# Performance work log

Measured on AMD Instinct MI355X. Metric: run time of the kernel, lower is better.

The kernel has to match this reference:

```python
import jax, jax.numpy as jnp
import numpy as np

B, S, E, H = 4, 1024, 768, 12
DH = E // H  # per-head dim = 64
PRIOR_VAR = 0.01


def _kl(mu, logvar):
    # kl_regularizer from the source: logvar (units,) broadcasts against mu (in,units)
    t = (jnp.log(PRIOR_VAR) - 1.0 - logvar
         + jnp.log1p(jnp.exp(logvar)) / PRIOR_VAR
         + mu * mu / PRIOR_VAR)
    return 0.5 * jnp.mean(t)


def _linear_first(x, w_mu, w_sigma):
    mu = x @ w_mu
    W_Sigma = jnp.log1p(jnp.exp(w_sigma))            # softplus(w_sigma)
    xs = x / x.shape[-1]                              # x / dim (dim = last dim of x)
    xx = jnp.sum(xs * xs, axis=-1, keepdims=True)     # [B,S,1]
    Sigma = jax.nn.softplus(xx * W_Sigma)             # [B,S,E]
    return mu, Sigma, _kl(w_mu, w_sigma)


def _linear_not_first(mu_in, Sigma_in, w_mu, w_sigma):
    mu = mu_in @ w_mu
    W_Sigma = jnp.log1p(jnp.exp(w_sigma))
    wm = w_mu / jnp.sqrt(jnp.float32(w_mu.shape[0]))  # w_mu / sqrt(in_dim)
    S1 = Sigma_in @ (wm * wm)                         # w^T Sigma_in w
    xs = mu_in / mu_in.shape[-1]
    S2 = jnp.sum(xs * xs, axis=-1, keepdims=True) * W_Sigma
    S3 = jnp.sum(Sigma_in, axis=-1, keepdims=True) * W_Sigma / W_Sigma.shape[-1]
    Sigma = jax.nn.softplus(S1 + S2 + S3)
    return mu, Sigma, _kl(w_mu, w_sigma)


def _heads(x):
    # [B,S,E] -> [B,H,S,DH]
    return x.reshape(B, S, H, DH).transpose(0, 2, 1, 3)


def setup_inputs() -> dict:
    key = jax.random.key(0)
    ks = jax.random.split(key, 9)
    glorot = lambda k: jax.random.normal(k, (E, E), jnp.float32) * jnp.sqrt(2.0 / (E + E))
    sig = lambda k: jax.random.uniform(k, (E,), jnp.float32, minval=-4.6, maxval=-2.25)
    return {
        "x": jax.random.normal(ks[0], (B, S, E), jnp.float32),
        "wq_mu": glorot(ks[1]), "wq_sigma": sig(ks[2]),
        "wk_mu": glorot(ks[3]), "wk_sigma": sig(ks[4]),
        "wv_mu": glorot(ks[5]), "wv_sigma": sig(ks[6]),
        "wo_mu": glorot(ks[7]), "wo_sigma": sig(ks[8]),
    }


def reference(x, wq_mu, wq_sigma, wk_mu, wk_sigma, wv_mu, wv_sigma, wo_mu, wo_sigma):
    # dropout is identity in eval mode (training=False)
    mq, sq, klq = _linear_first(x, wq_mu, wq_sigma)
    mk, sk, klk = _linear_first(x, wk_mu, wk_sigma)
    mv, sv, klv = _linear_first(x, wv_mu, wv_sigma)
    mq, sq, mk, sk, mv, sv = map(_heads, (mq, sq, mk, sk, mv, sv))

    dk = jnp.float32(DH)
    mu_score = jnp.einsum('bhqd,bhkd->bhqk', mq, mk)
    a = jnp.einsum('bhqd,bhkd->bhqk', mq * mq / dk, sk)
    b = jnp.einsum('bhqd,bhkd->bhqk', mk * mk / dk, sq)   # matmul(mk^2/dk, sq^T) as in TF source
    c = jnp.einsum('bhqd,bhkd->bhqk', sq / jnp.sqrt(dk), sk / jnp.sqrt(dk))
    sigma_score = a + b + c

    mu_scaled = mu_score / jnp.sqrt(dk)
    sigma_scaled = sigma_score / dk
    w = jax.nn.softmax(mu_scaled, axis=-1)               # [B,H,S,S]
    wd = jnp.float32(S)
    grad = (w - w * w) ** 2
    Sw = grad * sigma_scaled / wd

    mu_att = jnp.einsum('bhqk,bhkd->bhqd', w, mv)
    d = jnp.einsum('bhqk,bhkd->bhqd', w * w / wd, sv)
    e = jnp.einsum('bhqk,bhkd->bhqd', Sw, mv * mv / wd)
    f = jnp.einsum('bhqk,bhkd->bhqd', Sw / jnp.sqrt(wd), sv / jnp.sqrt(wd))
    sig_att = jax.nn.softplus(d + e + f)

    mu_cat = mu_att.transpose(0, 2, 1, 3).reshape(B, S, E)
    sig_cat = sig_att.transpose(0, 2, 1, 3).reshape(B, S, E)

    mu_out, Sigma_out, klo = _linear_not_first(mu_cat, sig_cat, wo_mu, wo_sigma)
    Sigma_out = jax.nn.softplus(Sigma_out)               # extra softplus in call()
    kl = klq + klk + klv + klo
    return mu_out, Sigma_out, kl
```

## Files before the change

kernel.cpp:

```cpp
#include <hip/hip_runtime.h>
#include <math.h>

#define EN 768
#define SN 1024
#define HN 12
#define BSN 4096
#define BSE 3145728

typedef __attribute__((ext_vector_type(8))) short bf16x8;
typedef __attribute__((ext_vector_type(4))) float f32x4;
typedef __attribute__((ext_vector_type(4))) unsigned short u16x4;
typedef __attribute__((ext_vector_type(4))) unsigned int u32x4;
typedef unsigned short u16;

#define OFF_XX   0u
#define OFF_RC   16384u
#define OFF_WSIG 32768u
#define OFF_KL   45056u
#define OFF_ZI   49152u
#define OFF_WT   262144u
#define OFF_QH   4980736u
#define OFF_KH   11272192u
#define OFF_SQD  17563648u
#define OFF_SKD  23855104u
#define OFF_MVT  30146560u
#define OFF_MV2  36438016u
#define OFF_SVT  42729472u
#define OFF_MUH  49020928u
#define OFF_SGH  55312384u

__device__ __forceinline__ float sp_f(float x){
  return fmaxf(x, 0.f) + log1pf(__expf(-fabsf(x)));
}
__device__ __forceinline__ u16 f2b(float f){
  unsigned u = __float_as_uint(f);
  return (u16)((u + 0x7fffu + ((u>>16)&1u)) >> 16);
}
__device__ __forceinline__ float b2f(u16 h){
  return __uint_as_float(((unsigned)h)<<16);
}
__device__ __forceinline__ unsigned cvtpk(float lo, float hi){
  unsigned r;
  asm("v_cvt_pk_bf16_f32 %0, %1, %2" : "=v"(r) : "v"(lo), "v"(hi));
  return r;
}
__device__ __forceinline__ bf16x8 u2b(u32x4 v){
  union{u32x4 u; bf16x8 b;} x; x.u = v; return x.b;
}
__device__ __forceinline__ f32x4 mfma16(bf16x8 a, bf16x8 b, f32x4 c){
  return __builtin_amdgcn_mfma_f32_16x16x32_bf16(a, b, c, 0, 0, 0);
}
__device__ __forceinline__ bf16x8 sq8(bf16x8 a){
  union{bf16x8 b; u32x4 u;} x; x.b = a;
  u32x4 r;
  #pragma unroll
  for (int i=0;i<4;++i){
    unsigned v = x.u[i];
    float f0 = __uint_as_float(v<<16);
    float f1 = __uint_as_float(v & 0xffff0000u);
    r[i] = cvtpk(f0*f0, f1*f1);
  }
  return u2b(r);
}
__device__ __forceinline__ bf16x8 ldsr(const u16* t, int row, int sg){
  int a16 = (row<<3) + (sg ^ (row&7));
  return *(const bf16x8*)(t + (a16<<3));
}
__device__ __forceinline__ void stage64(u16* dst, const u16* src, int rstride, int tid){
  #pragma unroll
  for (int it=0; it<2; ++it){
    int idx = (it<<8) + tid;
    int row = idx>>3, seg = idx&7;
    bf16x8 v = *(const bf16x8*)(src + (long)row*rstride + (seg<<3));
    int a16 = (row<<3) + (seg ^ (row&7));
    *(bf16x8*)(dst + (a16<<3)) = v;
  }
}

__device__ __forceinline__ float blk_reduce(float v, float* tmp){
  #pragma unroll
  for (int off = 32; off; off >>= 1) v += __shfl_down(v, off, 64);
  int w = threadIdx.x >> 6;
  if ((threadIdx.x & 63) == 0) tmp[w] = v;
  __syncthreads();
  float r = 0.f;
  if (threadIdx.x == 0) r = tmp[0] + tmp[1] + tmp[2] + tmp[3];
  __syncthreads();
  return r;
}

__global__ void k_prep(const float* __restrict__ s0, const float* __restrict__ s1,
                       const float* __restrict__ s2, const float* __restrict__ s3,
                       float* __restrict__ wsig, float* __restrict__ klacc){
  __shared__ float tmp[4];
  const float* src = (blockIdx.x==0)?s0:(blockIdx.x==1)?s1:(blockIdx.x==2)?s2:s3;
  int l = blockIdx.x;
  float ssum=0.f, spsum=0.f;
  for (int j=threadIdx.x; j<EN; j+=256){
    float sg = src[j];
    float w  = log1pf(__expf(sg));
    wsig[l*EN+j] = w;
    ssum += sg; spsum += w;
  }
  float a = blk_reduce(ssum, tmp);
  float b = blk_reduce(spsum, tmp);
  if (threadIdx.x==0){ atomicAdd(&klacc[1], a); atomicAdd(&klacc[2], b); }
}

__global__ void k_xx(const float* __restrict__ x, float* __restrict__ xx){
  __shared__ float tmp[4];
  int r = blockIdx.x;
  const float* xr = x + (long)r*EN;
  float s=0.f;
  for (int j=threadIdx.x; j<EN; j+=256){ float v = xr[j]; s += v*v; }
  float t = blk_reduce(s, tmp);
  if (threadIdx.x==0) xx[r] = t*(1.0f/589824.0f);
}

__global__ void k_mu2(const float* __restrict__ w0, const float* __restrict__ w1,
                      const float* __restrict__ w2, const float* __restrict__ w3,
                      float* __restrict__ klacc){
  __shared__ float tmp[4];
  const float* w = (blockIdx.y==0)?w0:(blockIdx.y==1)?w1:(blockIdx.y==2)?w2:w3;
  const float4* w4 = (const float4*)w;
  float s=0.f;
  for (int i=blockIdx.x*256+threadIdx.x; i<147456; i+=gridDim.x*256){
    float4 v = w4[i];
    s += v.x*v.x + v.y*v.y + v.z*v.z + v.w*v.w;
  }
  float r = blk_reduce(s, tmp);
  if (threadIdx.x==0) atomicAdd(&klacc[0], r);
}

__global__ void k_wt(const float* __restrict__ w0, const float* __restrict__ w1,
                     const float* __restrict__ w2, const float* __restrict__ w3,
                     u16* __restrict__ wt){
  __shared__ float t[64*65];
  const float* W = (blockIdx.z==0)?w0:(blockIdx.z==1)?w1:(blockIdx.z==2)?w2:w3;
  u16* WT = wt + (long)blockIdx.z*589824;
  int r0 = blockIdx.y<<6, c0 = blockIdx.x<<6;
  int tid = threadIdx.x;
  #pragma unroll
  for (int it=0; it<16; ++it){
    int idx=(it<<8)+tid; int r=idx>>6, c=idx&63;
    t[c*65+r] = W[(long)(r0+r)*EN + c0+c];
  }
  __syncthreads();
  #pragma unroll
  for (int it=0; it<16; ++it){
    int idx=(it<<8)+tid; int c=idx>>6, r=idx&63;
    WT[(long)(c0+c)*EN + r0+r] = f2b(t[c*65+r]);
  }
}

__global__ void k_sigarr(const float* __restrict__ xx, const float* __restrict__ wsig,
                         u16* __restrict__ sqd, u16* __restrict__ skd){
  int r = blockIdx.x;
  float xr = xx[r];
  for (int c=threadIdx.x; c<EN; c+=256){
    sqd[(long)r*EN+c] = f2b(sp_f(xr*wsig[c])*(1.0f/64.0f));
    skd[(long)r*EN+c] = f2b(sp_f(xr*wsig[EN+c])*(1.0f/64.0f));
  }
}

__global__ void k_svt(const float* __restrict__ xx, const float* __restrict__ wsig,
                      u16* __restrict__ svT){
  __shared__ float sxx[64], swv[64];
  int kt=blockIdx.x, h=blockIdx.y, b=blockIdx.z, tid=threadIdx.x;
  if (tid < 64){
    sxx[tid] = xx[(long)b*SN + (kt<<6) + tid];
    swv[tid] = wsig[2*EN + (h<<6) + tid];
  }
  __syncthreads();
  long obase = (((long)(b*HN+h))<<6)*SN + (kt<<6);
  #pragma unroll
  for (int it=0; it<16; ++it){
    int idx=(it<<8)+tid; int d=idx>>6, k=idx&63;
    svT[obase + (long)d*SN + k] = f2b(sp_f(sxx[k]*swv[d]));
  }
}

__global__ __launch_bounds__(256)
void k_projmm(const float* __restrict__ x, const u16* __restrict__ WT,
              u16* __restrict__ oq, u16* __restrict__ ok,
              u16* __restrict__ mvT, u16* __restrict__ mv2T){
  __shared__ __align__(16) u16 lds[8192];
  u16* At = lds; u16* Bt = lds + 4096;
  const int tid = threadIdx.x;
  const int w = tid>>6, l = tid&63, l15 = l&15, g = l>>4;
  const int m0 = blockIdx.y<<6, n0 = blockIdx.x<<6;
  const u16* Wt = WT + (long)blockIdx.z*589824;
  f32x4 acc[4];
  #pragma unroll
  for (int t=0;t<4;++t){ acc[t][0]=0;acc[t][1]=0;acc[t][2]=0;acc[t][3]=0; }
  for (int k0=0; k0<EN; k0+=64){
    __syncthreads();
    #pragma unroll
    for (int it=0; it<2; ++it){
      int idx=(it<<8)+tid; int row=idx>>3, seg=idx&7;
      const float* sp = x + (long)(m0+row)*EN + k0 + (seg<<3);
      float4 a = *(const float4*)sp; float4 c = *(const float4*)(sp+4);
      bf16x8 v;
      v[0]=(short)f2b(a.x); v[1]=(short)f2b(a.y); v[2]=(short)f2b(a.z); v[3]=(short)f2b(a.w);
      v[4]=(short)f2b(c.x); v[5]=(short)f2b(c.y); v[6]=(short)f2b(c.z); v[7]=(short)f2b(c.w);
      int a16=(row<<3)+(seg^(row&7));
      *(bf16x8*)(At + (a16<<3)) = v;
    }
    stage64(Bt, Wt + (long)n0*EN + k0, EN, tid);
    __syncthreads();
    #pragma unroll
    for (int s=0;s<2;++s){
      int sg=(s<<2)+g;
      bf16x8 af = ldsr(At, (w<<4)+l15, sg);
      #pragma unroll
      for (int t=0;t<4;++t)
        acc[t] = mfma16(af, ldsr(Bt,(t<<4)+l15,sg), acc[t]);
    }
  }
  if (blockIdx.z < 2){
    u16* out = blockIdx.z ? ok : oq;
    #pragma unroll
    for (int t=0;t<4;++t){
      int col = n0 + (t<<4) + l15;
      #pragma unroll
      for (int r=0;r<4;++r){
        long row = m0 + (w<<4) + (g<<2) + r;
        out[row*EN + col] = f2b(acc[t][r]);
      }
    }
  } else {
    int b  = m0 >> 10;
    int hh = n0 >> 6;
    long obase = (((long)(b*HN+hh))<<6)*SN;
    int tok0 = (m0 & 1023) + (w<<4) + (g<<2);
    #pragma unroll
    for (int t=0;t<4;++t){
      int d = (t<<4) + l15;
      u16x4 m4, s4;
      #pragma unroll
      for (int r=0;r<4;++r){
        u16 mb = f2b(acc[t][r]);
        m4[r] = mb;
        float mf = b2f(mb);
        s4[r] = f2b(mf*mf);
      }
      *(u16x4*)&mvT[obase + (long)d*SN + tok0]  = m4;
      *(u16x4*)&mv2T[obase + (long)d*SN + tok0] = s4;
    }
  }
}

__global__ __launch_bounds__(512)
void k_z(const u16* __restrict__ qh, const u16* __restrict__ kh,
         float* __restrict__ zi){
  __shared__ __align__(16) u16 Tk[4096];
  const int tid = threadIdx.x;
  const int w = tid>>6, l = tid&63, l15 = l&15, g = l>>4;
  const int i = blockIdx.x;
  const int xcd = i & 7, slot = i >> 3;
  const int qt = slot & 7;
  const int pair = xcd*6 + (slot >> 3);
  const int h = pair % HN, b = pair / HN;
  const int q0 = qt<<7;
  const long bS = (long)b*SN;
  bf16x8 amq[2];
  {
    long qrow = (bS + q0 + (w<<4) + l15) * EN;
    #pragma unroll
    for (int s=0;s<2;++s)
      amq[s] = *(const bf16x8*)(qh + qrow + (h<<6) + (s<<5) + (g<<3));
  }
  const u16* khb = kh + bS*EN + (h<<6);
  const int srow = tid>>3, sseg = tid&7;
  const int a16o = (((srow<<3) + (sseg ^ (srow&7)))<<3);
  bf16x8 pf = *(const bf16x8*)(khb + (long)srow*EN + (sseg<<3));
  f32x4 zacc = {0.f,0.f,0.f,0.f};
  for (int kt=0; kt<16; ++kt){
    __syncthreads();
    *(bf16x8*)(Tk + a16o) = pf;
    __syncthreads();
    if (kt < 15)
      pf = *(const bf16x8*)(khb + (long)(((kt+1)<<6)+srow)*EN + (sseg<<3));
    f32x4 smu[4];
    #pragma unroll
    for (int t=0;t<4;++t){ smu[t][0]=0;smu[t][1]=0;smu[t][2]=0;smu[t][3]=0; }
    #pragma unroll
    for (int s=0;s<2;++s){
      int sg=(s<<2)+g;
      #pragma unroll
      for (int t=0;t<4;++t)
        smu[t] = mfma16(amq[s], ldsr(Tk,(t<<4)+l15,sg), smu[t]);
    }
    #pragma unroll
    for (int t=0;t<4;++t)
      #pragma unroll
      for (int r=0;r<4;++r)
        zacc[r] += __expf(smu[t][r]*0.125f);
  }
  #pragma unroll
  for (int m=1; m<16; m<<=1){
    #pragma unroll
    for (int r=0;r<4;++r) zacc[r] += __shfl_xor(zacc[r], m, 64);
  }
  if (l15 == 0){
    long zbase = (((long)(b*HN+h))<<10) + q0 + (w<<4) + (g<<2);
    #pragma unroll
    for (int r=0;r<4;++r) zi[zbase + r] = 1.0f/zacc[r];
  }
}

__global__ __launch_bounds__(512, 2)
void k_attn(const u16* __restrict__ qh, const u16* __restrict__ kh,
            const u16* __restrict__ sqd, const u16* __restrict__ skd,
            const u16* __restrict__ mvT, const u16* __restrict__ svT,
            const u16* __restrict__ mv2T, const float* __restrict__ zi,
            u16* __restrict__ muh, u16* __restrict__ sgh){
  extern __shared__ u16 lds2[];
  u16* Tk  = lds2;
  u16* Tsk = lds2 + 4096;
  u16* Tsq = lds2 + 8192;
  u16* Tmv = lds2 + 12288;
  u16* Tsv = lds2 + 16384;
  u16* Tm2 = lds2 + 20480;
  const int tid = threadIdx.x;
  const int w = tid>>6, l = tid&63, l15 = l&15, g = l>>4;
  unsigned* Pu = (unsigned*)(lds2 + 24576) + (w<<10);
  const int i = blockIdx.x;
  const int xcd = i & 7, slot = i >> 3;
  const int qt = slot & 7;
  const int pair = xcd*6 + (slot >> 3);
  const int h = pair % HN, b = pair / HN;
  const int q0 = qt<<7;
  const long bS = (long)b*SN;

  bf16x8 amq[2], acb[2], amk2[2];
  {
    long qrow = (bS + q0 + (w<<4) + l15) * EN;
    #pragma unroll
    for (int s=0;s<2;++s){
      int eoff = (h<<6) + (s<<5) + (g<<3);
      bf16x8 q8 = *(const bf16x8*)(qh + qrow + eoff);
      bf16x8 k8 = *(const bf16x8*)(kh + qrow + eoff);
      bf16x8 s8 = *(const bf16x8*)(sqd + qrow + eoff);
      amq[s] = q8;
      bf16x8 t2, tc;
      #pragma unroll
      for (int j=0;j<8;++j){
        float kv = b2f((u16)k8[j]);
        t2[j] = (short)f2b(kv*kv);
        float qv = b2f((u16)q8[j]);
        float sv = b2f((u16)s8[j]) * 64.0f;
        tc[j] = (short)f2b(qv*qv + sv);
      }
      amk2[s] = t2; acb[s] = tc;
    }
  }
  float zl[4];
  {
    long zbase = (((long)(b*HN+h))<<10) + q0 + (w<<4) + (g<<2);
    #pragma unroll
    for (int r=0;r<4;++r) zl[r] = zi[zbase + r];
  }

  const u16* khb = kh  + bS*EN + (h<<6);
  const u16* skb = skd + bS*EN + (h<<6);
  const u16* sqb = sqd + bS*EN + (h<<6);
  const long hb64 = ((long)(b*HN+h))<<6;
  const u16* mvb = mvT  + hb64*SN;
  const u16* svb = svT  + hb64*SN;
  const u16* m2b = mv2T + hb64*SN;

  f32x4 accM[4], acc2[4], acc3[4];
  #pragma unroll
  for (int t=0;t<4;++t){
    accM[t][0]=0;accM[t][1]=0;accM[t][2]=0;accM[t][3]=0;
    acc2[t][0]=0;acc2[t][1]=0;acc2[t][2]=0;acc2[t][3]=0;
    acc3[t][0]=0;acc3[t][1]=0;acc3[t][2]=0;acc3[t][3]=0;
  }

  const int srow = tid>>3, sseg = tid&7;
  const int a16o = (((srow<<3) + (sseg ^ (srow&7)))<<3);

  bf16x8 pf0, pf1, pf2, pf3, pf4, pf5;
  {
    long off1 = (long)srow*EN + (sseg<<3);
    long off2 = (long)srow*SN + (sseg<<3);
    pf0 = *(const bf16x8*)(khb+off1);
    pf1 = *(const bf16x8*)(skb+off1);
    pf2 = *(const bf16x8*)(sqb+off1);
    pf3 = *(const bf16x8*)(mvb+off2);
    pf4 = *(const bf16x8*)(svb+off2);
    pf5 = *(const bf16x8*)(m2b+off2);
  }

  for (int kt=0; kt<16; ++kt){
    __syncthreads();
    *(bf16x8*)(Tk +a16o) = pf0;
    *(bf16x8*)(Tsk+a16o) = pf1;
    *(bf16x8*)(Tsq+a16o) = pf2;
    *(bf16x8*)(Tmv+a16o) = pf3;
    *(bf16x8*)(Tsv+a16o) = pf4;
    *(bf16x8*)(Tm2+a16o) = pf5;
    __syncthreads();
    if (kt < 15){
      long off1 = (long)(((kt+1)<<6)+srow)*EN + (sseg<<3);
      long off2 = (long)srow*SN + ((kt+1)<<6) + (sseg<<3);
      pf0 = *(const bf16x8*)(khb+off1);
      pf1 = *(const bf16x8*)(skb+off1);
      pf2 = *(const bf16x8*)(sqb+off1);
      pf3 = *(const bf16x8*)(mvb+off2);
      pf4 = *(const bf16x8*)(svb+off2);
      pf5 = *(const bf16x8*)(m2b+off2);
    }

    #pragma unroll
    for (int t=0;t<4;++t){
      f32x4 smu = {0.f,0.f,0.f,0.f}, ssg = {0.f,0.f,0.f,0.f};
      #pragma unroll
      for (int s=0;s<2;++s){
        int sg=(s<<2)+g;
        int rn = (t<<4)+l15;
        smu = mfma16(amq[s],  ldsr(Tk, rn,sg), smu);
        ssg = mfma16(acb[s],  ldsr(Tsk,rn,sg), ssg);
        ssg = mfma16(amk2[s], ldsr(Tsq,rn,sg), ssg);
      }
      #pragma unroll
      for (int r=0;r<4;++r){
        float e  = __expf(smu[r]*0.125f);
        float wv = e*zl[r];
        float u  = wv - wv*wv;
        float sw = u*u*ssg[r]*(1.0f/65536.0f);
        int prow = (g<<2)+r, pcol = (t<<4)+l15;
        int a32 = (((prow<<3) + ((pcol>>3)^(prow&7)))<<3) + (pcol&7);
        Pu[a32] = cvtpk(wv, sw);
      }
    }
    asm volatile("s_waitcnt lgkmcnt(0)" ::: "memory");
    #pragma unroll
    for (int s=0;s<2;++s){
      int sg=(s<<2)+g;
      const u32x4* pp = (const u32x4*)(Pu + (((l15<<3) + (sg ^ (l15&7)))<<3));
      u32x4 pA = pp[0], pB = pp[1];
      unsigned qa[8] = {pA[0],pA[1],pA[2],pA[3],pB[0],pB[1],pB[2],pB[3]};
      u32x4 awu, agu, pau;
      #pragma unroll
      for (int i2=0;i2<4;++i2){
        unsigned lo = qa[2*i2], hi = qa[2*i2+1];
        awu[i2] = (lo & 0xffffu) | (hi << 16);
        agu[i2] = (lo >> 16) | (hi & 0xffff0000u);
        float w0 = __uint_as_float(lo<<16), g0 = __uint_as_float(lo & 0xffff0000u);
        float w1 = __uint_as_float(hi<<16), g1 = __uint_as_float(hi & 0xffff0000u);
        pau[i2] = cvtpk(fmaf(w0,w0,g0), fmaf(w1,w1,g1));
      }
      bf16x8 aw = u2b(awu), ag = u2b(agu), pa = u2b(pau);
      #pragma unroll
      for (int t=0;t<4;++t){
        int rn = (t<<4)+l15;
        accM[t] = mfma16(aw, ldsr(Tmv,rn,sg), accM[t]);
        acc2[t] = mfma16(pa, ldsr(Tsv,rn,sg), acc2[t]);
        acc3[t] = mfma16(ag, ldsr(Tm2,rn,sg), acc3[t]);
      }
    }
  }
  long grow0 = bS + q0 + (w<<4) + (g<<2);
  #pragma unroll
  for (int t=0;t<4;++t){
    int col = (h<<6) + (t<<4) + l15;
    #pragma unroll
    for (int r=0;r<4;++r){
      long o = (grow0 + r)*EN + col;
      muh[o] = f2b(accM[t][r]);
      sgh[o] = f2b(sp_f((acc2[t][r]+acc3[t][r])*(1.0f/1024.0f)));
    }
  }
}

__global__ void k_rows(const u16* __restrict__ muh, const u16* __restrict__ sgh,
                       float* __restrict__ rcomb){
  __shared__ float tmp[4];
  int r = blockIdx.x;
  const u16* m = muh + (long)r*EN;
  const u16* s = sgh + (long)r*EN;
  float s1=0.f, s2=0.f;
  for (int j=threadIdx.x; j<EN; j+=256){ float a=b2f(m[j]); s1+=a*a; s2+=b2f(s[j]); }
  float r1 = blk_reduce(s1, tmp);
  float r2 = blk_reduce(s2, tmp);
  if (threadIdx.x==0) rcomb[r] = r1*(1.0f/589824.0f) + r2*(1.0f/768.0f);
}

__global__ __launch_bounds__(256)
void k_outmm(const u16* __restrict__ muh, const u16* __restrict__ sgh,
             const u16* __restrict__ WTo, const float* __restrict__ rcomb,
             const float* __restrict__ wso, float* __restrict__ mu_out,
             float* __restrict__ sg_out){
  __shared__ __align__(16) u16 lds[12288];
  u16* Am = lds; u16* As = lds + 4096; u16* Bt = lds + 8192;
  const int tid = threadIdx.x;
  const int w = tid>>6, l = tid&63, l15 = l&15, g = l>>4;
  const int m0 = blockIdx.y<<6, n0 = blockIdx.x<<6;
  f32x4 accM[4], accS[4];
  #pragma unroll
  for (int t=0;t<4;++t){
    accM[t][0]=0;accM[t][1]=0;accM[t][2]=0;accM[t][3]=0;
    accS[t][0]=0;accS[t][1]=0;accS[t][2]=0;accS[t][3]=0;
  }
  for (int k0=0; k0<EN; k0+=64){
    __syncthreads();
    stage64(Am, muh + (long)m0*EN + k0, EN, tid);
    stage64(As, sgh + (long)m0*EN + k0, EN, tid);
    stage64(Bt, WTo + (long)n0*EN + k0, EN, tid);
    __syncthreads();
    #pragma unroll
    for (int s=0;s<2;++s){
      int sg=(s<<2)+g;
      bf16x8 am = ldsr(Am, (w<<4)+l15, sg);
      bf16x8 as = ldsr(As, (w<<4)+l15, sg);
      #pragma unroll
      for (int t=0;t<4;++t){
        bf16x8 bw = ldsr(Bt,(t<<4)+l15,sg);
        accM[t] = mfma16(am, bw, accM[t]);
        accS[t] = mfma16(as, sq8(bw), accS[t]);
      }
    }
  }
  float rc4[4];
  #pragma unroll
  for (int r=0;r<4;++r) rc4[r] = rcomb[m0 + (w<<4) + (g<<2) + r];
  #pragma unroll
  for (int t=0;t<4;++t){
    int col = n0 + (t<<4) + l15;
    float wsc = wso[col];
    #pragma unroll
    for (int r=0;r<4;++r){
      long row = m0 + (w<<4) + (g<<2) + r;
      mu_out[row*EN + col] = accM[t][r];
      float spre = accS[t][r]*(1.0f/768.0f) + rc4[r]*wsc;
      sg_out[row*EN + col] = sp_f(sp_f(spre));
    }
  }
}

__global__ void k_klf(const float* __restrict__ klacc, float* __restrict__ out){
  float Smu2 = klacc[0], Ssig = klacc[1], Ssp = klacc[2];
  const float C = -5.60517018599f;
  out[0] = 0.5f*(4.f*C - Ssig*(1.0f/768.0f) + Ssp*(1.0f/7.68f) + Smu2*(1.0f/5898.24f));
}

extern "C" void kernel_launch(void* const* d_in, const int* in_sizes, int n_in,
                              void* d_out, int out_size, void* d_ws, size_t ws_size,
                              hipStream_t stream) {
  (void)in_sizes; (void)n_in; (void)out_size; (void)ws_size;
  const float* x      = (const float*)d_in[0];
  const float* wq_mu  = (const float*)d_in[1];
  const float* wq_sig = (const float*)d_in[2];
  const float* wk_mu  = (const float*)d_in[3];
  const float* wk_sig = (const float*)d_in[4];
  const float* wv_mu  = (const float*)d_in[5];
  const float* wv_sig = (const float*)d_in[6];
  const float* wo_mu  = (const float*)d_in[7];
  const float* wo_sig = (const float*)d_in[8];

  char* wsb = (char*)d_ws;
  float* xx    = (float*)(wsb + OFF_XX);
  float* rc    = (float*)(wsb + OFF_RC);
  float* wsig  = (float*)(wsb + OFF_WSIG);
  float* kla   = (float*)(wsb + OFF_KL);
  float* zi    = (float*)(wsb + OFF_ZI);
  u16*   WT    = (u16*)(wsb + OFF_WT);
  u16*   qh    = (u16*)(wsb + OFF_QH);
  u16*   kh    = (u16*)(wsb + OFF_KH);
  u16*   sqd   = (u16*)(wsb + OFF_SQD);
  u16*   skd   = (u16*)(wsb + OFF_SKD);
  u16*   mvT   = (u16*)(wsb + OFF_MVT);
  u16*   mv2T  = (u16*)(wsb + OFF_MV2);
  u16*   svT   = (u16*)(wsb + OFF_SVT);
  u16*   muh   = (u16*)(wsb + OFF_MUH);
  u16*   sgh   = (u16*)(wsb + OFF_SGH);

  float* mu_out = (float*)d_out;
  float* sg_out = mu_out + BSE;
  float* kl_out = mu_out + 2*BSE;

  (void)hipMemsetAsync(kla, 0, 3*sizeof(float), stream);
  k_prep<<<4, 256, 0, stream>>>(wq_sig, wk_sig, wv_sig, wo_sig, wsig, kla);
  k_xx<<<BSN, 256, 0, stream>>>(x, xx);
  k_mu2<<<dim3(64,4), 256, 0, stream>>>(wq_mu, wk_mu, wv_mu, wo_mu, kla);
  k_wt<<<dim3(12,12,4), 256, 0, stream>>>(wq_mu, wk_mu, wv_mu, wo_mu, WT);
  k_sigarr<<<BSN, 256, 0, stream>>>(xx, wsig, sqd, skd);
  k_svt<<<dim3(16,HN,4), 256, 0, stream>>>(xx, wsig, svT);
  k_projmm<<<dim3(12,64,3), 256, 0, stream>>>(x, WT, qh, kh, mvT, mv2T);
  k_z<<<384, 512, 0, stream>>>(qh, kh, zi);

  const int attn_lds = 40960*2;
  (void)hipFuncSetAttribute((const void*)k_attn,
                      hipFuncAttributeMaxDynamicSharedMemorySize, attn_lds);
  k_attn<<<384, 512, attn_lds, stream>>>(qh, kh, sqd, skd, mvT, svT,
                                         mv2T, zi, muh, sgh);
  k_rows<<<BSN, 256, 0, stream>>>(muh, sgh, rc);
  k_outmm<<<dim3(12,64), 256, 0, stream>>>(muh, sgh, WT + 3l*589824, rc,
                                           wsig + 3*EN, mu_out, sg_out);
  k_klf<<<1, 1, 0, stream>>>(kla, kl_out);
}
```

Measured before the change: 359.2 us.

## Halve attention waves with two q-subtiles per wave, direct global-to-LDS loads, precomputed squared Wo

The attention kernel now runs 256 threads per block. Each wave computes two 16-row query subtiles, so every B fragment read from LDS feeds twice as many MFMAs. Register-staged prefetch is replaced with global_load_lds direct copies, and the K/Sk/Sq loads for the next tile are issued after the score phase. Separately, k_wt writes a bf16 squared copy of Wo, so the output GEMM stages that copy instead of squaring every fragment in the inner loop. The cost is more accumulator registers per wave, fewer waves to hide latency, and extra LDS and global traffic for the squared-weight tile.

```diff
diff --git a/kernel.cpp b/kernel.cpp
--- a/kernel.cpp
+++ b/kernel.cpp
@@ -6,6 +6,9 @@
 #define HN 12
 #define BSN 4096
 #define BSE 3145728
+
+#define AS1 __attribute__((address_space(1)))
+#define AS3 __attribute__((address_space(3)))
 
 typedef __attribute__((ext_vector_type(8))) short bf16x8;
 typedef __attribute__((ext_vector_type(4))) float f32x4;
@@ -28,6 +31,7 @@
 #define OFF_SVT  42729472u
 #define OFF_MUH  49020928u
 #define OFF_SGH  55312384u
+#define OFF_WT2  61603840u
 
 __device__ __forceinline__ float sp_f(float x){
   return fmaxf(x, 0.f) + log1pf(__expf(-fabsf(x)));
@@ -49,18 +53,6 @@
 }
 __device__ __forceinline__ f32x4 mfma16(bf16x8 a, bf16x8 b, f32x4 c){
   return __builtin_amdgcn_mfma_f32_16x16x32_bf16(a, b, c, 0, 0, 0);
-}
-__device__ __forceinline__ bf16x8 sq8(bf16x8 a){
-  union{bf16x8 b; u32x4 u;} x; x.b = a;
-  u32x4 r;
-  #pragma unroll
-  for (int i=0;i<4;++i){
-    unsigned v = x.u[i];
-    float f0 = __uint_as_float(v<<16);
-    float f1 = __uint_as_float(v & 0xffff0000u);
-    r[i] = cvtpk(f0*f0, f1*f1);
-  }
-  return u2b(r);
 }
 __device__ __forceinline__ bf16x8 ldsr(const u16* t, int row, int sg){
   int a16 = (row<<3) + (sg ^ (row&7));
@@ -74,6 +66,18 @@
     bf16x8 v = *(const bf16x8*)(src + (long)row*rstride + (seg<<3));
     int a16 = (row<<3) + (seg ^ (row&7));
     *(bf16x8*)(dst + (a16<<3)) = v;
+  }
+}
+__device__ __forceinline__ void gstage(u16* ltile, const u16* gsrc, long rstride,
+                                       int w, int l){
+  #pragma unroll
+  for (int i=0;i<2;++i){
+    int slot = (i<<8) + (w<<6) + l;
+    int row  = slot >> 3;
+    int seg  = (slot & 7) ^ (row & 7);
+    const u16* g = gsrc + (long)row*rstride + (seg<<3);
+    u16* d = ltile + (((i<<8) + (w<<6))<<3);
+    __builtin_amdgcn_global_load_lds((AS1 void*)g, (AS3 void*)d, 16, 0, 0);
   }
 }
 
@@ -134,7 +138,7 @@
 
 __global__ void k_wt(const float* __restrict__ w0, const float* __restrict__ w1,
                      const float* __restrict__ w2, const float* __restrict__ w3,
-                     u16* __restrict__ wt){
+                     u16* __restrict__ wt, u16* __restrict__ wt2){
   __shared__ float t[64*65];
   const float* W = (blockIdx.z==0)?w0:(blockIdx.z==1)?w1:(blockIdx.z==2)?w2:w3;
   u16* WT = wt + (long)blockIdx.z*589824;
@@ -149,7 +153,12 @@
   #pragma unroll
   for (int it=0; it<16; ++it){
     int idx=(it<<8)+tid; int c=idx>>6, r=idx&63;
-    WT[(long)(c0+c)*EN + r0+r] = f2b(t[c*65+r]);
+    u16 bb = f2b(t[c*65+r]);
+    WT[(long)(c0+c)*EN + r0+r] = bb;
+    if (blockIdx.z == 3){
+      float bf = b2f(bb);
+      wt2[(long)(c0+c)*EN + r0+r] = f2b(bf*bf);
+    }
   }
 }
 
@@ -309,7 +318,7 @@
   }
 }
 
-__global__ __launch_bounds__(512, 2)
+__global__ __launch_bounds__(256, 2)
 void k_attn(const u16* __restrict__ qh, const u16* __restrict__ kh,
             const u16* __restrict__ sqd, const u16* __restrict__ skd,
             const u16* __restrict__ mvT, const u16* __restrict__ svT,
@@ -324,25 +333,26 @@
   u16* Tm2 = lds2 + 20480;
   const int tid = threadIdx.x;
   const int w = tid>>6, l = tid&63, l15 = l&15, g = l>>4;
-  unsigned* Pu = (unsigned*)(lds2 + 24576) + (w<<10);
-  const int i = blockIdx.x;
-  const int xcd = i & 7, slot = i >> 3;
+  unsigned* Pu = (unsigned*)(lds2 + 24576) + (w<<11);
+  const int ib = blockIdx.x;
+  const int xcd = ib & 7, slot = ib >> 3;
   const int qt = slot & 7;
   const int pair = xcd*6 + (slot >> 3);
   const int h = pair % HN, b = pair / HN;
   const int q0 = qt<<7;
   const long bS = (long)b*SN;
 
-  bf16x8 amq[2], acb[2], amk2[2];
-  {
-    long qrow = (bS + q0 + (w<<4) + l15) * EN;
+  bf16x8 amq[2][2], acb[2][2], amk2[2][2];
+  #pragma unroll
+  for (int p=0;p<2;++p){
+    long qrow = (bS + q0 + (w<<5) + (p<<4) + l15) * EN;
     #pragma unroll
     for (int s=0;s<2;++s){
       int eoff = (h<<6) + (s<<5) + (g<<3);
       bf16x8 q8 = *(const bf16x8*)(qh + qrow + eoff);
       bf16x8 k8 = *(const bf16x8*)(kh + qrow + eoff);
       bf16x8 s8 = *(const bf16x8*)(sqd + qrow + eoff);
-      amq[s] = q8;
+      amq[p][s] = q8;
       bf16x8 t2, tc;
       #pragma unroll
       for (int j=0;j<8;++j){
@@ -352,14 +362,15 @@
         float sv = b2f((u16)s8[j]) * 64.0f;
         tc[j] = (short)f2b(qv*qv + sv);
       }
-      amk2[s] = t2; acb[s] = tc;
-    }
-  }
-  float zl[4];
-  {
-    long zbase = (((long)(b*HN+h))<<10) + q0 + (w<<4) + (g<<2);
-    #pragma unroll
-    for (int r=0;r<4;++r) zl[r] = zi[zbase + r];
+      amk2[p][s] = t2; acb[p][s] = tc;
+    }
+  }
+  f32x4 zl[2];
+  #pragma unroll
+  for (int p=0;p<2;++p){
+    long zbase = (((long)(b*HN+h))<<10) + q0 + (w<<5) + (p<<4) + (g<<2);
+    #pragma unroll
+    for (int r=0;r<4;++r) zl[p][r] = zi[zbase + r];
   }
 
   const u16* khb = kh  + bS*EN + (h<<6);
@@ -370,107 +381,117 @@
   const u16* svb = svT  + hb64*SN;
   const u16* m2b = mv2T + hb64*SN;
 
-  f32x4 accM[4], acc2[4], acc3[4];
-  #pragma unroll
-  for (int t=0;t<4;++t){
-    accM[t][0]=0;accM[t][1]=0;accM[t][2]=0;accM[t][3]=0;
-    acc2[t][0]=0;acc2[t][1]=0;acc2[t][2]=0;acc2[t][3]=0;
-    acc3[t][0]=0;acc3[t][1]=0;acc3[t][2]=0;acc3[t][3]=0;
-  }
-
-  const int srow = tid>>3, sseg = tid&7;
-  const int a16o = (((srow<<3) + (sseg ^ (srow&7)))<<3);
-
-  bf16x8 pf0, pf1, pf2, pf3, pf4, pf5;
-  {
-    long off1 = (long)srow*EN + (sseg<<3);
-    long off2 = (long)srow*SN + (sseg<<3);
-    pf0 = *(const bf16x8*)(khb+off1);
-    pf1 = *(const bf16x8*)(skb+off1);
-    pf2 = *(const bf16x8*)(sqb+off1);
-    pf3 = *(const bf16x8*)(mvb+off2);
-    pf4 = *(const bf16x8*)(svb+off2);
-    pf5 = *(const bf16x8*)(m2b+off2);
-  }
+  f32x4 accM[2][4], acc2[2][4], acc3[2][4];
+  #pragma unroll
+  for (int p=0;p<2;++p)
+    #pragma unroll
+    for (int t=0;t<4;++t){
+      accM[p][t][0]=0;accM[p][t][1]=0;accM[p][t][2]=0;accM[p][t][3]=0;
+      acc2[p][t][0]=0;acc2[p][t][1]=0;acc2[p][t][2]=0;acc2[p][t][3]=0;
+      acc3[p][t][0]=0;acc3[p][t][1]=0;acc3[p][t][2]=0;acc3[p][t][3]=0;
+    }
+
+  gstage(Tk,  khb, EN, w, l);
+  gstage(Tsk, skb, EN, w, l);
+  gstage(Tsq, sqb, EN, w, l);
 
   for (int kt=0; kt<16; ++kt){
     __syncthreads();
-    *(bf16x8*)(Tk +a16o) = pf0;
-    *(bf16x8*)(Tsk+a16o) = pf1;
-    *(bf16x8*)(Tsq+a16o) = pf2;
-    *(bf16x8*)(Tmv+a16o) = pf3;
-    *(bf16x8*)(Tsv+a16o) = pf4;
-    *(bf16x8*)(Tm2+a16o) = pf5;
-    __syncthreads();
-    if (kt < 15){
-      long off1 = (long)(((kt+1)<<6)+srow)*EN + (sseg<<3);
-      long off2 = (long)srow*SN + ((kt+1)<<6) + (sseg<<3);
-      pf0 = *(const bf16x8*)(khb+off1);
-      pf1 = *(const bf16x8*)(skb+off1);
-      pf2 = *(const bf16x8*)(sqb+off1);
-      pf3 = *(const bf16x8*)(mvb+off2);
-      pf4 = *(const bf16x8*)(svb+off2);
-      pf5 = *(const bf16x8*)(m2b+off2);
-    }
+    gstage(Tmv, mvb + (kt<<6), SN, w, l);
+    gstage(Tsv, svb + (kt<<6), SN, w, l);
+    gstage(Tm2, m2b + (kt<<6), SN, w, l);
 
     #pragma unroll
     for (int t=0;t<4;++t){
-      f32x4 smu = {0.f,0.f,0.f,0.f}, ssg = {0.f,0.f,0.f,0.f};
+      f32x4 smu[2], ssg[2];
+      #pragma unroll
+      for (int p=0;p<2;++p){
+        smu[p][0]=0;smu[p][1]=0;smu[p][2]=0;smu[p][3]=0;
+        ssg[p][0]=0;ssg[p][1]=0;ssg[p][2]=0;ssg[p][3]=0;
+      }
+      int rn = (t<<4)+l15;
       #pragma unroll
       for (int s=0;s<2;++s){
         int sg=(s<<2)+g;
-        int rn = (t<<4)+l15;
-        smu = mfma16(amq[s],  ldsr(Tk, rn,sg), smu);
-        ssg = mfma16(acb[s],  ldsr(Tsk,rn,sg), ssg);
-        ssg = mfma16(amk2[s], ldsr(Tsq,rn,sg), ssg);
-      }
-      #pragma unroll
-      for (int r=0;r<4;++r){
-        float e  = __expf(smu[r]*0.125f);
-        float wv = e*zl[r];
-        float u  = wv - wv*wv;
-        float sw = u*u*ssg[r]*(1.0f/65536.0f);
-        int prow = (g<<2)+r, pcol = (t<<4)+l15;
-        int a32 = (((prow<<3) + ((pcol>>3)^(prow&7)))<<3) + (pcol&7);
-        Pu[a32] = cvtpk(wv, sw);
-      }
-    }
-    asm volatile("s_waitcnt lgkmcnt(0)" ::: "memory");
+        bf16x8 bk = ldsr(Tk, rn, sg);
+        bf16x8 bs = ldsr(Tsk,rn, sg);
+        bf16x8 bq = ldsr(Tsq,rn, sg);
+        #pragma unroll
+        for (int p=0;p<2;++p){
+          smu[p] = mfma16(amq[p][s],  bk, smu[p]);
+          ssg[p] = mfma16(acb[p][s],  bs, ssg[p]);
+          ssg[p] = mfma16(amk2[p][s], bq, ssg[p]);
+        }
+      }
+      #pragma unroll
+      for (int p=0;p<2;++p){
+        #pragma unroll
+        for (int r=0;r<4;++r){
+          float e  = __expf(smu[p][r]*0.125f);
+          float wv = e*zl[p][r];
+          float u  = wv - wv*wv;
+          float sw = u*u*ssg[p][r]*(1.0f/65536.0f);
+          int prow = (g<<2)+r, pcol = (t<<4)+l15;
+          int a32 = (p<<10) + ((((prow<<3) + ((pcol>>3)^(prow&7)))<<3) + (pcol&7));
+          Pu[a32] = cvtpk(wv, sw);
+        }
+      }
+    }
+    __syncthreads();
+    if (kt < 15){
+      long o1 = (long)((kt+1)<<6)*EN;
+      gstage(Tk,  khb + o1, EN, w, l);
+      gstage(Tsk, skb + o1, EN, w, l);
+      gstage(Tsq, sqb + o1, EN, w, l);
+    }
     #pragma unroll
     for (int s=0;s<2;++s){
       int sg=(s<<2)+g;
-      const u32x4* pp = (const u32x4*)(Pu + (((l15<<3) + (sg ^ (l15&7)))<<3));
-      u32x4 pA = pp[0], pB = pp[1];
-      unsigned qa[8] = {pA[0],pA[1],pA[2],pA[3],pB[0],pB[1],pB[2],pB[3]};
-      u32x4 awu, agu, pau;
-      #pragma unroll
-      for (int i2=0;i2<4;++i2){
-        unsigned lo = qa[2*i2], hi = qa[2*i2+1];
-        awu[i2] = (lo & 0xffffu) | (hi << 16);
-        agu[i2] = (lo >> 16) | (hi & 0xffff0000u);
-        float w0 = __uint_as_float(lo<<16), g0 = __uint_as_float(lo & 0xffff0000u);
-        float w1 = __uint_as_float(hi<<16), g1 = __uint_as_float(hi & 0xffff0000u);
-        pau[i2] = cvtpk(fmaf(w0,w0,g0), fmaf(w1,w1,g1));
-      }
-      bf16x8 aw = u2b(awu), ag = u2b(agu), pa = u2b(pau);
+      bf16x8 aw[2], ag[2], pa[2];
+      #pragma unroll
+      for (int p=0;p<2;++p){
+        const u32x4* pp = (const u32x4*)(Pu + (p<<10) + (((l15<<3) + (sg ^ (l15&7)))<<3));
+        u32x4 pA = pp[0], pB = pp[1];
+        unsigned qa[8] = {pA[0],pA[1],pA[2],pA[3],pB[0],pB[1],pB[2],pB[3]};
+        u32x4 awu, agu, pau;
+        #pragma unroll
+        for (int i2=0;i2<4;++i2){
+          unsigned lo = qa[2*i2], hi = qa[2*i2+1];
+          awu[i2] = (lo & 0xffffu) | (hi << 16);
+          agu[i2] = (lo >> 16) | (hi & 0xffff0000u);
+          float w0 = __uint_as_float(lo<<16), g0 = __uint_as_float(lo & 0xffff0000u);
+          float w1 = __uint_as_float(hi<<16), g1 = __uint_as_float(hi & 0xffff0000u);
+          pau[i2] = cvtpk(fmaf(w0,w0,g0), fmaf(w1,w1,g1));
+        }
+        aw[p]=u2b(awu); ag[p]=u2b(agu); pa[p]=u2b(pau);
+      }
       #pragma unroll
       for (int t=0;t<4;++t){
         int rn = (t<<4)+l15;
-        accM[t] = mfma16(aw, ldsr(Tmv,rn,sg), accM[t]);
-        acc2[t] = mfma16(pa, ldsr(Tsv,rn,sg), acc2[t]);
-        acc3[t] = mfma16(ag, ldsr(Tm2,rn,sg), acc3[t]);
-      }
-    }
-  }
-  long grow0 = bS + q0 + (w<<4) + (g<<2);
-  #pragma unroll
-  for (int t=0;t<4;++t){
-    int col = (h<<6) + (t<<4) + l15;
-    #pragma unroll
-    for (int r=0;r<4;++r){
-      long o = (grow0 + r)*EN + col;
-      muh[o] = f2b(accM[t][r]);
-      sgh[o] = f2b(sp_f((acc2[t][r]+acc3[t][r])*(1.0f/1024.0f)));
+        bf16x8 bm  = ldsr(Tmv,rn,sg);
+        bf16x8 bv  = ldsr(Tsv,rn,sg);
+        bf16x8 b2m = ldsr(Tm2,rn,sg);
+        #pragma unroll
+        for (int p=0;p<2;++p){
+          accM[p][t] = mfma16(aw[p], bm,  accM[p][t]);
+          acc2[p][t] = mfma16(pa[p], bv,  acc2[p][t]);
+          acc3[p][t] = mfma16(ag[p], b2m, acc3[p][t]);
+        }
+      }
+    }
+  }
+  #pragma unroll
+  for (int p=0;p<2;++p){
+    long grow0 = bS + q0 + (w<<5) + (p<<4) + (g<<2);
+    #pragma unroll
+    for (int t=0;t<4;++t){
+      int col = (h<<6) + (t<<4) + l15;
+      #pragma unroll
+      for (int r=0;r<4;++r){
+        long o = (grow0 + r)*EN + col;
+        muh[o] = f2b(accM[p][t][r]);
+        sgh[o] = f2b(sp_f((acc2[p][t][r]+acc3[p][t][r])*(1.0f/1024.0f)));
+      }
     }
   }
 }
@@ -490,11 +511,11 @@
 
 __global__ __launch_bounds__(256)
 void k_outmm(const u16* __restrict__ muh, const u16* __restrict__ sgh,
-             const u16* __restrict__ WTo, const float* __restrict__ rcomb,
-             const float* __restrict__ wso, float* __restrict__ mu_out,
-             float* __restrict__ sg_out){
-  __shared__ __align__(16) u16 lds[12288];
-  u16* Am = lds; u16* As = lds + 4096; u16* Bt = lds + 8192;
+             const u16* __restrict__ WTo, const u16* __restrict__ WT2o,
+             const float* __restrict__ rcomb, const float* __restrict__ wso,
+             float* __restrict__ mu_out, float* __restrict__ sg_out){
+  __shared__ __align__(16) u16 lds[16384];
+  u16* Am = lds; u16* As = lds + 4096; u16* Bt = lds + 8192; u16* B2t = lds + 12288;
   const int tid = threadIdx.x;
   const int w = tid>>6, l = tid&63, l15 = l&15, g = l>>4;
   const int m0 = blockIdx.y<<6, n0 = blockIdx.x<<6;
@@ -509,6 +530,7 @@
     stage64(Am, muh + (long)m0*EN + k0, EN, tid);
     stage64(As, sgh + (long)m0*EN + k0, EN, tid);
     stage64(Bt, WTo + (long)n0*EN + k0, EN, tid);
+    stage64(B2t, WT2o + (long)n0*EN + k0, EN, tid);
     __syncthreads();
     #pragma unroll
     for (int s=0;s<2;++s){
@@ -517,9 +539,9 @@
       bf16x8 as = ldsr(As, (w<<4)+l15, sg);
       #pragma unroll
       for (int t=0;t<4;++t){
-        bf16x8 bw = ldsr(Bt,(t<<4)+l15,sg);
-        accM[t] = mfma16(am, bw, accM[t]);
-        accS[t] = mfma16(as, sq8(bw), accS[t]);
+        int rn=(t<<4)+l15;
+        accM[t] = mfma16(am, ldsr(Bt,rn,sg), accM[t]);
+        accS[t] = mfma16(as, ldsr(B2t,rn,sg), accS[t]);
       }
     }
   }
@@ -576,6 +598,7 @@
   u16*   svT   = (u16*)(wsb + OFF_SVT);
   u16*   muh   = (u16*)(wsb + OFF_MUH);
   u16*   sgh   = (u16*)(wsb + OFF_SGH);
+  u16*   WT2   = (u16*)(wsb + OFF_WT2);
 
   float* mu_out = (float*)d_out;
   float* sg_out = mu_out + BSE;
@@ -585,19 +608,19 @@
   k_prep<<<4, 256, 0, stream>>>(wq_sig, wk_sig, wv_sig, wo_sig, wsig, kla);
   k_xx<<<BSN, 256, 0, stream>>>(x, xx);
   k_mu2<<<dim3(64,4), 256, 0, stream>>>(wq_mu, wk_mu, wv_mu, wo_mu, kla);
-  k_wt<<<dim3(12,12,4), 256, 0, stream>>>(wq_mu, wk_mu, wv_mu, wo_mu, WT);
+  k_wt<<<dim3(12,12,4), 256, 0, stream>>>(wq_mu, wk_mu, wv_mu, wo_mu, WT, WT2);
   k_sigarr<<<BSN, 256, 0, stream>>>(xx, wsig, sqd, skd);
   k_svt<<<dim3(16,HN,4), 256, 0, stream>>>(xx, wsig, svT);
   k_projmm<<<dim3(12,64,3), 256, 0, stream>>>(x, WT, qh, kh, mvT, mv2T);
   k_z<<<384, 512, 0, stream>>>(qh, kh, zi);
 
-  const int attn_lds = 40960*2;
+  const int attn_lds = 81920;
   (void)hipFuncSetAttribute((const void*)k_attn,
                       hipFuncAttributeMaxDynamicSharedMemorySize, attn_lds);
-  k_attn<<<384, 512, attn_lds, stream>>>(qh, kh, sqd, skd, mvT, svT,
+  k_attn<<<384, 256, attn_lds, stream>>>(qh, kh, sqd, skd, mvT, svT,
                                          mv2T, zi, muh, sgh);
   k_rows<<<BSN, 256, 0, stream>>>(muh, sgh, rc);
-  k_outmm<<<dim3(12,64), 256, 0, stream>>>(muh, sgh, WT + 3l*589824, rc,
+  k_outmm<<<dim3(12,64), 256, 0, stream>>>(muh, sgh, WT + 3l*589824, WT2, rc,
                                            wsig + 3*EN, mu_out, sg_out);
   k_klf<<<1, 1, 0, stream>>>(kla, kl_out);
 }
```

After: 341.6 us. -4.9%, faster.
